# Performance work log

Measured on AMD Instinct MI355X. Metric: run time of the kernel, lower is better.

## Reference

```python
import jax, jax.numpy as jnp
import numpy as np

COMMITMENT_COST = 0.25

def _l2norm(v, axis=-1, eps=1e-12):
    # matches F.normalize(p=2): v / max(||v||, eps)
    n = jnp.sqrt(jnp.sum(v * v, axis=axis, keepdims=True))
    return v / jnp.maximum(n, eps)

def setup_inputs() -> dict:
    key = jax.random.key(0)
    k1, k2 = jax.random.split(key)
    N, D, K = 131072, 64, 2048
    x = jax.random.normal(k1, (N, D), dtype=jnp.float32)
    embeddings = jax.random.normal(k2, (K, D), dtype=jnp.float32)
    return {"x": x, "embeddings": embeddings}

def reference(x, embeddings):
    # x: [N, D] latents; embeddings: [K, D] codebook
    xn = _l2norm(x, axis=-1)                 # [N, D]
    en = _l2norm(embeddings, axis=-1)        # [K, D]
    # squared euclidean distances: ||xn||^2 + ||en||^2 - 2 xn.en
    d = (jnp.sum(xn * xn, axis=-1, keepdims=True)
         + jnp.sum(en * en, axis=-1)[None, :]
         - 2.0 * jnp.einsum('nd,kd->nk', xn, en))   # [N, K]
    idx = jnp.argmin(d, axis=1)              # [N] int
    quantized = en[idx]                      # [N, D] (already unit-norm; re-normalizing is idempotent but matches quantize())
    quantized = _l2norm(quantized, axis=-1)
    q_latent_loss = jnp.mean((quantized - jax.lax.stop_gradient(xn)) ** 2)
    e_latent_loss = jnp.mean((xn - jax.lax.stop_gradient(quantized)) ** 2)
    loss = q_latent_loss + COMMITMENT_COST * e_latent_loss
    # straight-through estimator
    quantized_st = xn + jax.lax.stop_gradient(quantized - xn)
    return quantized_st, loss, idx
```

## Files before the change

kernel.cpp:

```cpp
#include <hip/hip_runtime.h>
#include <math.h>
#include <stdint.h>


#define D 64
#define EPS 1e-12f
#define WPB 4
#define RG 2
#define RPW (RG * 16)
#define RPB (WPB * RPW)
#define CAP 832
#define MARGIN 0.010f

typedef short bf16x8 __attribute__((ext_vector_type(8)));
typedef float f32x4 __attribute__((ext_vector_type(4)));

__device__ __forceinline__ uint32_t f2bf(float f) {
    uint32_t u = __builtin_bit_cast(uint32_t, f);
    return (u + 0x7FFFu + ((u >> 16) & 1u)) >> 16;
}
__device__ __forceinline__ int xsw(int row, int d) {
    return row * 64 + ((((d >> 2) ^ (row & 7)) << 2) | (d & 3));
}

__global__ __launch_bounds__(1024) void vq_prep(const float* __restrict__ emb,
                                                float* __restrict__ en,
                                                float* __restrict__ en2,
                                                uint32_t* __restrict__ frags,
                                                float* __restrict__ loss_out,
                                                int K) {
    __shared__ float sh[16][64];
    int w = (int)(threadIdx.x >> 6), lane = (int)(threadIdx.x & 63);
    int tile = (int)blockIdx.x;
    int row = tile * 16 + w;
    if (row < K) {
        float v = emb[(size_t)row * D + lane];
        float s = v * v;
        #pragma unroll
        for (int m = 32; m >= 1; m >>= 1) s += __shfl_xor(s, m, 64);
        float e = v / fmaxf(sqrtf(s), EPS);
        float s2 = e * e;
        #pragma unroll
        for (int m = 32; m >= 1; m >>= 1) s2 += __shfl_xor(s2, m, 64);
        en[(size_t)row * D + lane] = e;
        if (lane == 0) en2[row] = s2;
        sh[w][lane] = e;
    }
    if (blockIdx.x == 0 && threadIdx.x == 0) loss_out[0] = 0.f;
    __syncthreads();
    if (w == 0) {
        int cl = lane & 15, dbase = (lane >> 4) * 8;
        #pragma unroll
        for (int h = 0; h < 2; ++h) {
            const float* p = &sh[cl][h * 32 + dbase];
            uint4 u;
            u.x = f2bf(p[0]) | (f2bf(p[1]) << 16);
            u.y = f2bf(p[2]) | (f2bf(p[3]) << 16);
            u.z = f2bf(p[4]) | (f2bf(p[5]) << 16);
            u.w = f2bf(p[6]) | (f2bf(p[7]) << 16);
            *(uint4*)(frags + ((size_t)(tile * 2 + h) * 64 + lane) * 4) = u;
        }
    }
}

__global__ __launch_bounds__(256, 4) void vq_main(const float* __restrict__ x,
                                                  const float* __restrict__ en,
                                                  const float* __restrict__ en2g,
                                                  const uint32_t* __restrict__ frags,
                                                  float* __restrict__ out_q,
                                                  float* __restrict__ out_idx,
                                                  float* __restrict__ loss_out,
                                                  int N, int K) {
    __shared__ float xn[RPB * 64];
    __shared__ uint16_t cand[WPB][CAP];
    __shared__ int candcnt[WPB];
    __shared__ unsigned long long keys[RPB];
    __shared__ double red[WPB];

    const int tid = (int)threadIdx.x;
    const int w = tid >> 6, lane = tid & 63;
    const int rowbase = (int)blockIdx.x * RPB;
    const int NT = K / 16;
    const int lq = (lane >> 4) << 2;

    for (int r = 0; r < RPW; ++r) {
        int rb = w * RPW + r;
        float v = x[(size_t)(rowbase + rb) * D + lane];
        float s = v * v;
        #pragma unroll
        for (int m = 32; m >= 1; m >>= 1) s += __shfl_xor(s, m, 64);
        xn[xsw(rb, lane)] = v / fmaxf(sqrtf(s), EPS);
    }
    if (lane == 0) candcnt[w] = 0;
    if (lane < RPW) keys[w * RPW + lane] = ~0ull;

    bf16x8 bfr[RG][2];
    #pragma unroll
    for (int g = 0; g < RG; ++g)
        #pragma unroll
        for (int h = 0; h < 2; ++h) {
            int row = w * RPW + g * 16 + (lane & 15);
            int db = h * 32 + ((lane >> 4) * 8);
            union { uint32_t u[4]; bf16x8 v; } cvt;
            #pragma unroll
            for (int j = 0; j < 4; ++j)
                cvt.u[j] = f2bf(xn[xsw(row, db + 2 * j)]) |
                           (f2bf(xn[xsw(row, db + 2 * j + 1)]) << 16);
            bfr[g][h] = cvt.v;
        }

    float runmax[RG];
    #pragma unroll
    for (int g = 0; g < RG; ++g) runmax[g] = -3.0e38f;
    const f32x4 zero4 = {0.f, 0.f, 0.f, 0.f};

    auto score = [&](int T, bf16x8 A0, bf16x8 A1) {
        int cb = T * 16 + lq;
        f32x4 acc[RG];
        #pragma unroll
        for (int g = 0; g < RG; ++g) {
            acc[g] = __builtin_amdgcn_mfma_f32_16x16x32_bf16(A0, bfr[g][0], zero4, 0, 0, 0);
            acc[g] = __builtin_amdgcn_mfma_f32_16x16x32_bf16(A1, bfr[g][1], acc[g], 0, 0, 0);
        }
        #pragma unroll
        for (int g = 0; g < RG; ++g) {
            float m4 = fmaxf(fmaxf(acc[g][0], acc[g][1]), fmaxf(acc[g][2], acc[g][3]));
            float rm = fmaxf(m4, __shfl_xor(m4, 16, 64));
            rm = fmaxf(rm, __shfl_xor(rm, 32, 64));
            runmax[g] = fmaxf(runmax[g], rm);
            float tau = runmax[g] - MARGIN;
            if (__any(m4 >= tau)) {
                int rloc = g * 16 + (lane & 15);
                #pragma unroll
                for (int q = 0; q < 4; ++q) {
                    if (acc[g][q] >= tau) {
                        int k = cb + q;
                        int slot = atomicAdd(&candcnt[w], 1);
                        if (slot < CAP) {
                            cand[w][slot] = (uint16_t)((k << 5) | rloc);
                        } else {
                            const float* ev = en + (size_t)k * D;
                            float dot = 0.f;
                            #pragma unroll
                            for (int d0 = 0; d0 < D; ++d0)
                                dot = fmaf(xn[xsw(w * RPW + rloc, d0)], ev[d0], dot);
                            float R = fmaf(-0.5f, en2g[k], dot);
                            uint32_t fb = __builtin_bit_cast(uint32_t, -R);
                            uint32_t ord = (fb & 0x80000000u) ? ~fb : (fb | 0x80000000u);
                            atomicMin(&keys[w * RPW + rloc],
                                      ((unsigned long long)ord << 32) | (uint32_t)k);
                        }
                    }
                }
            }
        }
    };

    const bf16x8* p = (const bf16x8*)frags + lane;
    bf16x8 A0 = p[0], A1 = p[64];
    for (int t = 0; t < NT; t += 2) {
        bf16x8 B0 = p[128], B1 = p[192];
        score(t, A0, A1);
        if (t + 2 < NT) { A0 = p[256]; A1 = p[320]; }
        score(t + 1, B0, B1);
        p += 256;
        if (((t + 1) & 15) == 15) __syncthreads();
    }

    int cnt = candcnt[w];
    cnt = cnt < CAP ? cnt : CAP;
    for (int base = 0; base < cnt; base += 64) {
        int i = base + lane;
        if (i < cnt) {
            uint32_t e = cand[w][i];
            int k = (int)(e >> 5), rloc = (int)(e & 31u);
            const float* ev = en + (size_t)k * D;
            float dot = 0.f;
            #pragma unroll
            for (int d0 = 0; d0 < D; ++d0)
                dot = fmaf(xn[xsw(w * RPW + rloc, d0)], ev[d0], dot);
            float R = fmaf(-0.5f, en2g[k], dot);
            uint32_t fb = __builtin_bit_cast(uint32_t, -R);
            uint32_t ord = (fb & 0x80000000u) ? ~fb : (fb | 0x80000000u);
            atomicMin(&keys[w * RPW + rloc],
                      ((unsigned long long)ord << 32) | (uint32_t)k);
        }
    }

    float ls = 0.f;
    for (int r = 0; r < RPW; ++r) {
        int rb = w * RPW + r;
        int k = (int)(keys[rb] & 0x7FFull);
        float rn = fmaxf(sqrtf(en2g[k]), EPS);
        float q = en[(size_t)k * D + lane] / rn;
        float a = xn[xsw(rb, lane)];
        float dx = q - a;
        ls = fmaf(dx, dx, ls);
        out_q[(size_t)(rowbase + rb) * D + lane] = a + dx;
    }
    if (lane < RPW) out_idx[rowbase + w * RPW + lane] =
        (float)(int)(keys[w * RPW + lane] & 0x7FFull);
    #pragma unroll
    for (int m = 32; m >= 1; m >>= 1) ls += __shfl_xor(ls, m, 64);
    if (lane == 0) red[w] = (double)ls;
    __syncthreads();
    if (tid == 0) {
        double s = 0.0;
        #pragma unroll
        for (int i = 0; i < WPB; ++i) s += red[i];
        atomicAdd(loss_out, (float)(s * (1.25 / ((double)N * (double)D))));
    }
}

extern "C" void kernel_launch(void* const* d_in, const int* in_sizes, int n_in,
                              void* d_out, int out_size, void* d_ws, size_t ws_size,
                              hipStream_t stream) {
    const float* x   = (const float*)d_in[0];
    const float* emb = (const float*)d_in[1];
    int N = in_sizes[0] / D;
    int K = in_sizes[1] / D;

    float* out      = (float*)d_out;
    float* out_q    = out;
    float* loss_out = out + (size_t)N * D;
    float* out_idx  = out + (size_t)N * D + 1;

    char* ws = (char*)d_ws;
    float*    en2   = (float*)(ws + 8192);
    float*    en    = (float*)(ws + 16384);
    uint32_t* frags = (uint32_t*)(ws + 540672);

    vq_prep<<<K / 16, 1024, 0, stream>>>(emb, en, en2, frags, loss_out, K);
    vq_main<<<N / RPB, 256, 0, stream>>>(x, en, en2, frags, out_q, out_idx,
                                         loss_out, N, K);
}
```

Before: 184.2 us.

## Split scoring into max-finding pass and candidate-collection pass over codebook

Replaces the single-pass running-max candidate filter with two passes. The first pass computes the bf16 MFMA scores and tracks only per-row maxima. The second recomputes the scores against the final threshold, so far fewer candidates pass and get refined in fp32. This doubles the MFMA and fragment-load work in exchange for removing the shuffle reductions and the wasted candidate appends in the hot loop.

```diff
diff --git a/kernel.cpp b/kernel.cpp
--- a/kernel.cpp
+++ b/kernel.cpp
@@ -109,62 +109,86 @@
             bfr[g][h] = cvt.v;
         }
 
-    float runmax[RG];
-    #pragma unroll
-    for (int g = 0; g < RG; ++g) runmax[g] = -3.0e38f;
     const f32x4 zero4 = {0.f, 0.f, 0.f, 0.f};
-
-    auto score = [&](int T, bf16x8 A0, bf16x8 A1) {
-        int cb = T * 16 + lq;
-        f32x4 acc[RG];
-        #pragma unroll
-        for (int g = 0; g < RG; ++g) {
-            acc[g] = __builtin_amdgcn_mfma_f32_16x16x32_bf16(A0, bfr[g][0], zero4, 0, 0, 0);
-            acc[g] = __builtin_amdgcn_mfma_f32_16x16x32_bf16(A1, bfr[g][1], acc[g], 0, 0, 0);
-        }
-        #pragma unroll
-        for (int g = 0; g < RG; ++g) {
-            float m4 = fmaxf(fmaxf(acc[g][0], acc[g][1]), fmaxf(acc[g][2], acc[g][3]));
-            float rm = fmaxf(m4, __shfl_xor(m4, 16, 64));
-            rm = fmaxf(rm, __shfl_xor(rm, 32, 64));
-            runmax[g] = fmaxf(runmax[g], rm);
-            float tau = runmax[g] - MARGIN;
-            if (__any(m4 >= tau)) {
-                int rloc = g * 16 + (lane & 15);
+    const bf16x8* fb = (const bf16x8*)frags + lane;
+
+    f32x4 rmax[RG];
+    #pragma unroll
+    for (int g = 0; g < RG; ++g) rmax[g] = {-3.0e38f, -3.0e38f, -3.0e38f, -3.0e38f};
+    {
+        const bf16x8* p = fb;
+        bf16x8 A0 = p[0], A1 = p[64];
+        for (int t = 0; t < NT; t += 2) {
+            bf16x8 B0 = p[128], B1 = p[192];
+            #pragma unroll
+            for (int g = 0; g < RG; ++g) {
+                f32x4 acc = __builtin_amdgcn_mfma_f32_16x16x32_bf16(A0, bfr[g][0], zero4, 0, 0, 0);
+                acc = __builtin_amdgcn_mfma_f32_16x16x32_bf16(A1, bfr[g][1], acc, 0, 0, 0);
                 #pragma unroll
-                for (int q = 0; q < 4; ++q) {
-                    if (acc[g][q] >= tau) {
-                        int k = cb + q;
-                        int slot = atomicAdd(&candcnt[w], 1);
-                        if (slot < CAP) {
-                            cand[w][slot] = (uint16_t)((k << 5) | rloc);
-                        } else {
-                            const float* ev = en + (size_t)k * D;
-                            float dot = 0.f;
-                            #pragma unroll
-                            for (int d0 = 0; d0 < D; ++d0)
-                                dot = fmaf(xn[xsw(w * RPW + rloc, d0)], ev[d0], dot);
-                            float R = fmaf(-0.5f, en2g[k], dot);
-                            uint32_t fb = __builtin_bit_cast(uint32_t, -R);
-                            uint32_t ord = (fb & 0x80000000u) ? ~fb : (fb | 0x80000000u);
-                            atomicMin(&keys[w * RPW + rloc],
-                                      ((unsigned long long)ord << 32) | (uint32_t)k);
+                for (int q = 0; q < 4; ++q) rmax[g][q] = fmaxf(rmax[g][q], acc[q]);
+            }
+            if (t + 2 < NT) { A0 = p[256]; A1 = p[320]; }
+            #pragma unroll
+            for (int g = 0; g < RG; ++g) {
+                f32x4 acc = __builtin_amdgcn_mfma_f32_16x16x32_bf16(B0, bfr[g][0], zero4, 0, 0, 0);
+                acc = __builtin_amdgcn_mfma_f32_16x16x32_bf16(B1, bfr[g][1], acc, 0, 0, 0);
+                #pragma unroll
+                for (int q = 0; q < 4; ++q) rmax[g][q] = fmaxf(rmax[g][q], acc[q]);
+            }
+            p += 256;
+            if (((t + 1) & 15) == 15) __syncthreads();
+        }
+    }
+    float tau[RG];
+    #pragma unroll
+    for (int g = 0; g < RG; ++g) {
+        float m = fmaxf(fmaxf(rmax[g][0], rmax[g][1]), fmaxf(rmax[g][2], rmax[g][3]));
+        m = fmaxf(m, __shfl_xor(m, 16, 64));
+        m = fmaxf(m, __shfl_xor(m, 32, 64));
+        tau[g] = m - MARGIN;
+    }
+
+    {
+        const bf16x8* p = fb;
+        bf16x8 A0 = p[0], A1 = p[64];
+        for (int t = 0; t < NT; ++t) {
+            bf16x8 nA0, nA1;
+            if (t + 1 < NT) { nA0 = p[128]; nA1 = p[192]; }
+            int cb = t * 16 + lq;
+            #pragma unroll
+            for (int g = 0; g < RG; ++g) {
+                f32x4 acc = __builtin_amdgcn_mfma_f32_16x16x32_bf16(A0, bfr[g][0], zero4, 0, 0, 0);
+                acc = __builtin_amdgcn_mfma_f32_16x16x32_bf16(A1, bfr[g][1], acc, 0, 0, 0);
+                float m4 = fmaxf(fmaxf(acc[0], acc[1]), fmaxf(acc[2], acc[3]));
+                if (__any(m4 >= tau[g])) {
+                    int rloc = g * 16 + (lane & 15);
+                    #pragma unroll
+                    for (int q = 0; q < 4; ++q) {
+                        if (acc[q] >= tau[g]) {
+                            int k = cb + q;
+                            int slot = atomicAdd(&candcnt[w], 1);
+                            if (slot < CAP) {
+                                cand[w][slot] = (uint16_t)((k << 5) | rloc);
+                            } else {
+                                const float* ev = en + (size_t)k * D;
+                                float dot = 0.f;
+                                #pragma unroll
+                                for (int d0 = 0; d0 < D; ++d0)
+                                    dot = fmaf(xn[xsw(w * RPW + rloc, d0)], ev[d0], dot);
+                                float R = fmaf(-0.5f, en2g[k], dot);
+                                uint32_t fbt = __builtin_bit_cast(uint32_t, -R);
+                                uint32_t ord = (fbt & 0x80000000u) ? ~fbt : (fbt | 0x80000000u);
+                                atomicMin(&keys[w * RPW + rloc],
+                                          ((unsigned long long)ord << 32) | (uint32_t)k);
+                            }
                         }
                     }
                 }
             }
-        }
-    };
-
-    const bf16x8* p = (const bf16x8*)frags + lane;
-    bf16x8 A0 = p[0], A1 = p[64];
-    for (int t = 0; t < NT; t += 2) {
-        bf16x8 B0 = p[128], B1 = p[192];
-        score(t, A0, A1);
-        if (t + 2 < NT) { A0 = p[256]; A1 = p[320]; }
-        score(t + 1, B0, B1);
-        p += 256;
-        if (((t + 1) & 15) == 15) __syncthreads();
+            A0 = nA0; A1 = nA1;
+            p += 128;
+            if ((t & 15) == 15) __syncthreads();
+        }
     }
 
     int cnt = candcnt[w];
@@ -180,8 +204,8 @@
             for (int d0 = 0; d0 < D; ++d0)
                 dot = fmaf(xn[xsw(w * RPW + rloc, d0)], ev[d0], dot);
             float R = fmaf(-0.5f, en2g[k], dot);
-            uint32_t fb = __builtin_bit_cast(uint32_t, -R);
-            uint32_t ord = (fb & 0x80000000u) ? ~fb : (fb | 0x80000000u);
+            uint32_t fbt = __builtin_bit_cast(uint32_t, -R);
+            uint32_t ord = (fbt & 0x80000000u) ? ~fbt : (fbt | 0x80000000u);
             atomicMin(&keys[w * RPW + rloc],
                       ((unsigned long long)ord << 32) | (uint32_t)k);
         }
```

After: 184.0 us. No clear change (-0.1%).
